# Performance work log

Measured on AMD Instinct MI355X. Metric: run time of the kernel, lower is better.

## Reference

```python
import jax, jax.numpy as jnp
import numpy as np

N, S, E, H = 2, 2048, 1024, 16
D = E // H  # size_per_head


def setup_inputs() -> dict:
    key = jax.random.key(0)
    ks = jax.random.split(key, 12)
    s = 0.02
    inp = {
        "key":   jax.random.normal(ks[0], (N, S, E), jnp.float32),
        "value": jax.random.normal(ks[1], (N, S, E), jnp.float32),
        "query": jax.random.normal(ks[2], (N, S, E), jnp.float32),
        # causal mask (S, T): 1 = attend, 0 = masked
        "mask":  jnp.tril(jnp.ones((S, S), jnp.int32)),
        "Wk": jax.random.normal(ks[3], (E, E), jnp.float32) * s,
        "bk": jnp.zeros((E,), jnp.float32),
        "Wq": jax.random.normal(ks[4], (E, E), jnp.float32) * s,
        "bq": jnp.zeros((E,), jnp.float32),
        "Wv": jax.random.normal(ks[5], (E, E), jnp.float32) * s,
        "bv": jnp.zeros((E,), jnp.float32),
        "Wp": jax.random.normal(ks[6], (E, E), jnp.float32) * s,
        "bp": jnp.zeros((E,), jnp.float32),
    }
    return inp


def _heads(x, W, b):
    # (N, L, E) -> (N, H, L, D)
    n, l, _ = x.shape
    y = x @ W.T + b
    return y.reshape(n, l, H, D).transpose(0, 2, 1, 3)


def reference(key, value, query, mask, Wk, bk, Wq, bq, Wv, bv, Wp, bp):
    q = _heads(query, Wq, bq)  # (N, H, S, D)
    k = _heads(key,   Wk, bk)  # (N, H, T, D)
    v = _heads(value, Wv, bv)  # (N, H, T, D)
    scale = 1.0 / jnp.sqrt(jnp.float32(D))
    scores = jnp.einsum("bhsd,bhtd->bhst", q, k) * scale  # (N, H, S, T)
    scores = jnp.where(mask == 0, jnp.float32(-1e12), scores)
    probs = jax.nn.softmax(scores, axis=-1)
    ctx = jnp.einsum("bhst,bhtd->bhsd", probs, v)  # (N, H, S, D)
    ctx = ctx.transpose(0, 2, 1, 3).reshape(query.shape[0], -1, E)  # (N, S, E)
    return ctx @ Wp.T + bp
```

## Files before the change

kernel.cpp:

```cpp
#include <hip/hip_runtime.h>
#include <hip/hip_bf16.h>
#include <math.h>

constexpr int N_B = 2;
constexpr int S_LEN = 2048;
constexpr int E_DIM = 1024;
constexpr int H_NUM = 16;
constexpr int D_HEAD = 64;
constexpr int M_ROWS = N_B * S_LEN;

#define Q_SCALE 0.180336880263082f

typedef __attribute__((ext_vector_type(8))) short bf16x8;
typedef __attribute__((ext_vector_type(4))) float f32x4;

__device__ __forceinline__ short f2bs(float x) {
    __hip_bfloat16 h = __float2bfloat16(x);
    return *reinterpret_cast<short*>(&h);
}

__device__ __forceinline__ void async_lds16(const void* g, void* l) {
    __builtin_amdgcn_global_load_lds(
        (const __attribute__((address_space(1))) unsigned int*)g,
        (__attribute__((address_space(3))) unsigned int*)l, 16, 0, 0);
}

__global__ __launch_bounds__(256) void cast_kernel(
    const float* __restrict__ a0, const float* __restrict__ a1, const float* __restrict__ a2,
    const float* __restrict__ a3, const float* __restrict__ a4, const float* __restrict__ a5,
    const float* __restrict__ a6,
    short* __restrict__ b0, short* __restrict__ b1, short* __restrict__ b2,
    short* __restrict__ b3, short* __restrict__ b4, short* __restrict__ b5,
    short* __restrict__ b6, int n8_in, int n8_w)
{
    const int y = blockIdx.y;
    const float* s; short* d;
    switch (y) {
        case 0: s = a0; d = b0; break;
        case 1: s = a1; d = b1; break;
        case 2: s = a2; d = b2; break;
        case 3: s = a3; d = b3; break;
        case 4: s = a4; d = b4; break;
        case 5: s = a5; d = b5; break;
        default: s = a6; d = b6; break;
    }
    const int n8 = (y < 3) ? n8_in : n8_w;
    const int i = blockIdx.x * 256 + threadIdx.x;
    if (i >= n8) return;
    const float4* f4 = (const float4*)s;
    const float4 a = f4[i * 2], b = f4[i * 2 + 1];
    bf16x8 o;
    o[0] = f2bs(a.x); o[1] = f2bs(a.y); o[2] = f2bs(a.z); o[3] = f2bs(a.w);
    o[4] = f2bs(b.x); o[5] = f2bs(b.y); o[6] = f2bs(b.z); o[7] = f2bs(b.w);
    *(bf16x8*)(d + (size_t)i * 8) = o;
}

__device__ __forceinline__ void gemm128_core(
    const short* __restrict__ A, const short* __restrict__ W,
    const float* __restrict__ bias, float* __restrict__ outf,
    short* __restrict__ outb, int mode, float scale, short* As, short* Bs)
{
    constexpr int K = E_DIM;
    const int tid = threadIdx.x;
    const int wave = tid >> 6, lane = tid & 63;
    const int l16 = lane & 15, quad = lane >> 4;
    const int wm = wave >> 1, wn = wave & 1;
    const int m0 = blockIdx.y * 128, n0 = blockIdx.x * 128;
    const int lr = lane >> 2;
    const int lc = (lane & 3) * 8;

    const short* Arow0 = A + (size_t)(m0 + wave * 16 + lr) * K + lc;
    const short* Arow1 = A + (size_t)(m0 + (wave + 4) * 16 + lr) * K + lc;
    const short* Wrow0 = W + (size_t)(n0 + wave * 16 + lr) * K + lc;
    const short* Wrow1 = W + (size_t)(n0 + (wave + 4) * 16 + lr) * K + lc;
    short* Asw0 = As + wave * 512; short* Asw1 = As + (wave + 4) * 512;
    short* Bsw0 = Bs + wave * 512; short* Bsw1 = Bs + (wave + 4) * 512;

    f32x4 acc[4][4];
    #pragma unroll
    for (int i = 0; i < 4; ++i)
        #pragma unroll
        for (int j = 0; j < 4; ++j)
            acc[i][j] = (f32x4){0.f, 0.f, 0.f, 0.f};

    for (int k0 = 0; k0 < K; k0 += 32) {
        async_lds16(Arow0 + k0, Asw0);
        async_lds16(Arow1 + k0, Asw1);
        async_lds16(Wrow0 + k0, Bsw0);
        async_lds16(Wrow1 + k0, Bsw1);
        __syncthreads();

        bf16x8 af[4], bfr[4];
        #pragma unroll
        for (int i = 0; i < 4; ++i) {
            af[i]  = *(const bf16x8*)(As + (wm * 64 + i * 16 + l16) * 32 + quad * 8);
            bfr[i] = *(const bf16x8*)(Bs + (wn * 64 + i * 16 + l16) * 32 + quad * 8);
        }
        #pragma unroll
        for (int mi = 0; mi < 4; ++mi)
            #pragma unroll
            for (int ni = 0; ni < 4; ++ni)
                acc[mi][ni] = __builtin_amdgcn_mfma_f32_16x16x32_bf16(
                    af[mi], bfr[ni], acc[mi][ni], 0, 0, 0);
        __syncthreads();
    }

    #pragma unroll
    for (int ni = 0; ni < 4; ++ni) {
        const int n = n0 + wn * 64 + ni * 16 + l16;
        const float bv = bias[n];
        #pragma unroll
        for (int mi = 0; mi < 4; ++mi) {
            #pragma unroll
            for (int r = 0; r < 4; ++r) {
                const int m = m0 + wm * 64 + mi * 16 + quad * 4 + r;
                const float val = (acc[mi][ni][r] + bv) * scale;
                if (mode == 0) {
                    outf[(size_t)m * E_DIM + n] = val;
                } else {
                    const int nb = m >> 11, s = m & 2047;
                    const int hh = n >> 6, d = n & 63;
                    if (mode == 1)
                        outb[(((size_t)(nb * H_NUM + hh)) * S_LEN + s) * D_HEAD + d] = f2bs(val);
                    else
                        outb[(((size_t)(nb * H_NUM + hh)) * D_HEAD + d) * S_LEN + s] = f2bs(val);
                }
            }
        }
    }
}

__global__ __launch_bounds__(256) void qkv_gemm_kernel(
    const short* __restrict__ qA, const short* __restrict__ kA, const short* __restrict__ vA,
    const short* __restrict__ Wq, const short* __restrict__ Wk, const short* __restrict__ Wv,
    const float* __restrict__ bq, const float* __restrict__ bk, const float* __restrict__ bv,
    short* __restrict__ oq, short* __restrict__ ok, short* __restrict__ ov)
{
    __shared__ short As[128 * 32];
    __shared__ short Bs[128 * 32];
    const int z = blockIdx.z;
    const short* A = z == 0 ? qA : z == 1 ? kA : vA;
    const short* W = z == 0 ? Wq : z == 1 ? Wk : Wv;
    const float* b = z == 0 ? bq : z == 1 ? bk : bv;
    short* o       = z == 0 ? oq : z == 1 ? ok : ov;
    gemm128_core(A, W, b, nullptr, o, z == 2 ? 2 : 1,
                 z == 0 ? Q_SCALE : 1.0f, As, Bs);
}

__global__ __launch_bounds__(256) void proj_gemm_kernel(
    const short* __restrict__ A, const short* __restrict__ W,
    const float* __restrict__ b, float* __restrict__ out)
{
    __shared__ short As[128 * 32];
    __shared__ short Bs[128 * 32];
    gemm128_core(A, W, b, out, nullptr, 0, 1.0f, As, Bs);
}

__global__ __launch_bounds__(256, 2) void fattn_kernel(
    const short* __restrict__ qg, const short* __restrict__ kg,
    const short* __restrict__ vtg, short* __restrict__ ctx)
{
    const int nh   = blockIdx.x & 31;
    const int pidx = blockIdx.x >> 5;
    const int tid  = threadIdx.x;
    const int wave = tid >> 6, lane = tid & 63;
    const int l16  = lane & 15, quad = lane >> 4;

    __shared__ short Ks[2][64 * 64];
    __shared__ short Vs[2][64 * 64];
    __shared__ short Ps[4][16 * 72];

    const size_t hb = (size_t)nh * S_LEN * D_HEAD;
    const short* kb  = kg + hb;
    const short* vtb = vtg + hb;
    const int nb = nh >> 4, h = nh & 15;

    const int srow = lane >> 3;
    const int schk = ((lane & 7) ^ srow) * 8;
    const int sw   = l16 & 7;

    for (int pi = 0; pi < 2; ++pi) {
        const int qt = pi ? (31 - pidx) : pidx;
        const int q0 = qt * 64;
        const int ntile = qt + 1;

        const short* qp = qg + hb + (size_t)(q0 + wave * 16 + l16) * D_HEAD;
        const bf16x8 qf0 = *(const bf16x8*)(qp + quad * 8);
        const bf16x8 qf1 = *(const bf16x8*)(qp + 32 + quad * 8);

        f32x4 O[4];
        float m_r[4], l_r[4];
        #pragma unroll
        for (int r = 0; r < 4; ++r) {
            O[r] = (f32x4){0.f, 0.f, 0.f, 0.f};
            m_r[r] = -1e30f;
            l_r[r] = 0.f;
        }
        const int qmaxw = q0 + wave * 16 + 15;

        __syncthreads();
        #pragma unroll
        for (int j = 0; j < 2; ++j) {
            const int r0 = wave * 16 + j * 8;
            async_lds16(kb + (size_t)(r0 + srow) * D_HEAD + schk, &Ks[0][r0 * 64]);
            async_lds16(vtb + (size_t)(r0 + srow) * S_LEN + schk, &Vs[0][r0 * 64]);
        }

        for (int it = 0; it < ntile; ++it) {
            const int buf = it & 1;
            const int t0 = it * 64;
            __syncthreads();

            if (it + 1 < ntile) {
                const int t1 = t0 + 64;
                #pragma unroll
                for (int j = 0; j < 2; ++j) {
                    const int r0 = wave * 16 + j * 8;
                    async_lds16(kb + (size_t)(t1 + r0 + srow) * D_HEAD + schk,
                                &Ks[buf ^ 1][r0 * 64]);
                    async_lds16(vtb + (size_t)(r0 + srow) * S_LEN + t1 + schk,
                                &Vs[buf ^ 1][r0 * 64]);
                }
            }

            const bool isdiag = (it == qt);

            float sc[4][4];
            #pragma unroll
            for (int c = 0; c < 4; ++c) {
                const bool act = !isdiag || (c <= wave);
                if (act) {
                    const int t = c * 16 + l16;
                    const bf16x8 k0 = *(const bf16x8*)(&Ks[buf][t * 64 + ((quad ^ sw) * 8)]);
                    const bf16x8 k1 = *(const bf16x8*)(&Ks[buf][t * 64 + (((quad + 4) ^ sw) * 8)]);
                    f32x4 s = {0.f, 0.f, 0.f, 0.f};
                    s = __builtin_amdgcn_mfma_f32_16x16x32_bf16(qf0, k0, s, 0, 0, 0);
                    s = __builtin_amdgcn_mfma_f32_16x16x32_bf16(qf1, k1, s, 0, 0, 0);
                    if (isdiag) {
                        const int tg = t0 + c * 16 + l16;
                        #pragma unroll
                        for (int r = 0; r < 4; ++r) {
                            const int qrow = q0 + wave * 16 + quad * 4 + r;
                            sc[c][r] = (tg <= qrow) ? s[r] : -1e30f;
                        }
                    } else {
                        #pragma unroll
                        for (int r = 0; r < 4; ++r) sc[c][r] = s[r];
                    }
                } else {
                    #pragma unroll
                    for (int r = 0; r < 4; ++r) sc[c][r] = -1e30f;
                }
            }

            float rmax[4];
            #pragma unroll
            for (int r = 0; r < 4; ++r)
                rmax[r] = fmaxf(fmaxf(sc[0][r], sc[1][r]), fmaxf(sc[2][r], sc[3][r]));
            #pragma unroll
            for (int off = 1; off < 16; off <<= 1)
                #pragma unroll
                for (int r = 0; r < 4; ++r)
                    rmax[r] = fmaxf(rmax[r], __shfl_xor(rmax[r], off));

            float alpha[4], p[4][4], rsum[4];
            #pragma unroll
            for (int r = 0; r < 4; ++r) {
                const float mn = fmaxf(m_r[r], rmax[r]);
                alpha[r] = __builtin_amdgcn_exp2f(m_r[r] - mn);
                m_r[r] = mn;
                #pragma unroll
                for (int c = 0; c < 4; ++c)
                    p[c][r] = __builtin_amdgcn_exp2f(sc[c][r] - mn);
                rsum[r] = (p[0][r] + p[1][r]) + (p[2][r] + p[3][r]);
            }
            #pragma unroll
            for (int off = 1; off < 16; off <<= 1)
                #pragma unroll
                for (int r = 0; r < 4; ++r)
                    rsum[r] += __shfl_xor(rsum[r], off);
            #pragma unroll
            for (int r = 0; r < 4; ++r)
                l_r[r] = l_r[r] * alpha[r] + rsum[r];

            #pragma unroll
            for (int c = 0; c < 4; ++c)
                #pragma unroll
                for (int r = 0; r < 4; ++r)
                    Ps[wave][(quad * 4 + r) * 72 + c * 16 + l16] = f2bs(p[c][r]);

            #pragma unroll
            for (int nt = 0; nt < 4; ++nt)
                #pragma unroll
                for (int r = 0; r < 4; ++r)
                    O[nt][r] *= alpha[r];

            const bf16x8 pf0 = *(const bf16x8*)(&Ps[wave][l16 * 72 + quad * 8]);
            const bf16x8 pf1 = *(const bf16x8*)(&Ps[wave][l16 * 72 + 32 + quad * 8]);
            #pragma unroll
            for (int nt = 0; nt < 4; ++nt) {
                const int d = nt * 16 + l16;
                const bf16x8 v0 = *(const bf16x8*)(&Vs[buf][d * 64 + ((quad ^ sw) * 8)]);
                const bf16x8 v1 = *(const bf16x8*)(&Vs[buf][d * 64 + (((quad + 4) ^ sw) * 8)]);
                O[nt] = __builtin_amdgcn_mfma_f32_16x16x32_bf16(pf0, v0, O[nt], 0, 0, 0);
                O[nt] = __builtin_amdgcn_mfma_f32_16x16x32_bf16(pf1, v1, O[nt], 0, 0, 0);
            }
        }

        float inv[4];
        #pragma unroll
        for (int r = 0; r < 4; ++r) inv[r] = 1.f / l_r[r];
        #pragma unroll
        for (int nt = 0; nt < 4; ++nt) {
            #pragma unroll
            for (int r = 0; r < 4; ++r) {
                const int qrow = q0 + wave * 16 + quad * 4 + r;
                const int d = nt * 16 + l16;
                ctx[((size_t)(nb * S_LEN + qrow)) * E_DIM + h * D_HEAD + d] =
                    f2bs(O[nt][r] * inv[r]);
            }
        }
    }
}

extern "C" void kernel_launch(void* const* d_in, const int* in_sizes, int n_in,
                              void* d_out, int out_size, void* d_ws, size_t ws_size,
                              hipStream_t stream) {
    const float* key   = (const float*)d_in[0];
    const float* value = (const float*)d_in[1];
    const float* query = (const float*)d_in[2];
    const float* Wk = (const float*)d_in[4];
    const float* bk = (const float*)d_in[5];
    const float* Wq = (const float*)d_in[6];
    const float* bq = (const float*)d_in[7];
    const float* Wv = (const float*)d_in[8];
    const float* bv = (const float*)d_in[9];
    const float* Wp = (const float*)d_in[10];
    const float* bp = (const float*)d_in[11];

    const size_t ielems = (size_t)M_ROWS * E_DIM;
    const size_t welems = (size_t)E_DIM * E_DIM;
    char* ws = (char*)d_ws;
    short* qib = (short*)(ws);
    short* kib = (short*)(ws + 8  * 1024 * 1024);
    short* vib = (short*)(ws + 16 * 1024 * 1024);
    short* Wqb = (short*)(ws + 24 * 1024 * 1024);
    short* Wkb = (short*)(ws + 26 * 1024 * 1024);
    short* Wvb = (short*)(ws + 28 * 1024 * 1024);
    short* Wpb = (short*)(ws + 30 * 1024 * 1024);
    short* qb  = (short*)(ws + 32 * 1024 * 1024);
    short* kb  = (short*)(ws + 40 * 1024 * 1024);
    short* vbt = (short*)(ws + 48 * 1024 * 1024);
    short* ctx = (short*)(ws + 56 * 1024 * 1024);
    float* out = (float*)d_out;

    cast_kernel<<<dim3((int)(ielems / 8 / 256), 7), 256, 0, stream>>>(
        query, key, value, Wq, Wk, Wv, Wp,
        qib, kib, vib, Wqb, Wkb, Wvb, Wpb,
        (int)(ielems / 8), (int)(welems / 8));

    qkv_gemm_kernel<<<dim3(E_DIM / 128, M_ROWS / 128, 3), 256, 0, stream>>>(
        qib, kib, vib, Wqb, Wkb, Wvb, bq, bk, bv, qb, kb, vbt);

    fattn_kernel<<<dim3(H_NUM * N_B * 16), 256, 0, stream>>>(qb, kb, vbt, ctx);

    proj_gemm_kernel<<<dim3(E_DIM / 128, M_ROWS / 128), 256, 0, stream>>>(
        ctx, Wpb, bp, out);
}
```

Before: 260.8 us.

## Double-buffer GEMM loads, shrink proj tile, transpose attention MFMA for per-lane rows

The GEMM core now double-buffers its LDS tiles, issuing the async global-to-LDS loads for the next K slice before computing on the current one, and drops one barrier per iteration. The projection GEMM uses a 64-row tile so more blocks are launched. The attention kernel swaps MFMA operand order so each lane owns one query row: the row max and sum need only two cross-lane shuffles, the diagonal mask is simpler, and P and ctx are written as packed 8-byte stores. In exchange, the GEMM kernels use twice the LDS, and the narrower proj tile reuses each loaded W tile across fewer rows.

```diff
diff --git a/kernel.cpp b/kernel.cpp
--- a/kernel.cpp
+++ b/kernel.cpp
@@ -17,6 +17,10 @@
 __device__ __forceinline__ short f2bs(float x) {
     __hip_bfloat16 h = __float2bfloat16(x);
     return *reinterpret_cast<short*>(&h);
+}
+__device__ __forceinline__ unsigned int pk2(float a, float b) {
+    return (unsigned int)(unsigned short)f2bs(a) |
+           ((unsigned int)(unsigned short)f2bs(b) << 16);
 }
 
 __device__ __forceinline__ void async_lds16(const void* g, void* l) {
@@ -55,54 +59,70 @@
     *(bf16x8*)(d + (size_t)i * 8) = o;
 }
 
-__device__ __forceinline__ void gemm128_core(
+template <int TM>
+__device__ __forceinline__ void gemm_core(
     const short* __restrict__ A, const short* __restrict__ W,
     const float* __restrict__ bias, float* __restrict__ outf,
     short* __restrict__ outb, int mode, float scale, short* As, short* Bs)
 {
     constexpr int K = E_DIM;
+    constexpr int MI = TM / 32;
     const int tid = threadIdx.x;
     const int wave = tid >> 6, lane = tid & 63;
     const int l16 = lane & 15, quad = lane >> 4;
     const int wm = wave >> 1, wn = wave & 1;
-    const int m0 = blockIdx.y * 128, n0 = blockIdx.x * 128;
+    const int m0 = blockIdx.y * TM, n0 = blockIdx.x * 128;
     const int lr = lane >> 2;
     const int lc = (lane & 3) * 8;
 
     const short* Arow0 = A + (size_t)(m0 + wave * 16 + lr) * K + lc;
-    const short* Arow1 = A + (size_t)(m0 + (wave + 4) * 16 + lr) * K + lc;
+    const short* Arow1 = A + (size_t)(m0 + ((TM == 128 ? wave + 4 : wave)) * 16 + lr) * K + lc;
     const short* Wrow0 = W + (size_t)(n0 + wave * 16 + lr) * K + lc;
     const short* Wrow1 = W + (size_t)(n0 + (wave + 4) * 16 + lr) * K + lc;
-    short* Asw0 = As + wave * 512; short* Asw1 = As + (wave + 4) * 512;
-    short* Bsw0 = Bs + wave * 512; short* Bsw1 = Bs + (wave + 4) * 512;
-
-    f32x4 acc[4][4];
+
+    f32x4 acc[MI][4];
     #pragma unroll
-    for (int i = 0; i < 4; ++i)
+    for (int i = 0; i < MI; ++i)
         #pragma unroll
         for (int j = 0; j < 4; ++j)
             acc[i][j] = (f32x4){0.f, 0.f, 0.f, 0.f};
 
+    {
+        short* Ab = As; short* Bb = Bs;
+        async_lds16(Arow0, Ab + wave * 512);
+        if (TM == 128) async_lds16(Arow1, Ab + (wave + 4) * 512);
+        async_lds16(Wrow0, Bb + wave * 512);
+        async_lds16(Wrow1, Bb + (wave + 4) * 512);
+    }
+
     for (int k0 = 0; k0 < K; k0 += 32) {
-        async_lds16(Arow0 + k0, Asw0);
-        async_lds16(Arow1 + k0, Asw1);
-        async_lds16(Wrow0 + k0, Bsw0);
-        async_lds16(Wrow1 + k0, Bsw1);
+        const int b = (k0 >> 5) & 1;
+        short* Ab = As + b * (TM * 32);
+        short* Bb = Bs + b * (128 * 32);
         __syncthreads();
 
-        bf16x8 af[4], bfr[4];
-        #pragma unroll
-        for (int i = 0; i < 4; ++i) {
-            af[i]  = *(const bf16x8*)(As + (wm * 64 + i * 16 + l16) * 32 + quad * 8);
-            bfr[i] = *(const bf16x8*)(Bs + (wn * 64 + i * 16 + l16) * 32 + quad * 8);
-        }
-        #pragma unroll
-        for (int mi = 0; mi < 4; ++mi)
+        if (k0 + 32 < K) {
+            short* An = As + (b ^ 1) * (TM * 32);
+            short* Bn = Bs + (b ^ 1) * (128 * 32);
+            async_lds16(Arow0 + k0 + 32, An + wave * 512);
+            if (TM == 128) async_lds16(Arow1 + k0 + 32, An + (wave + 4) * 512);
+            async_lds16(Wrow0 + k0 + 32, Bn + wave * 512);
+            async_lds16(Wrow1 + k0 + 32, Bn + (wave + 4) * 512);
+        }
+
+        bf16x8 af[MI], bfr[4];
+        #pragma unroll
+        for (int i = 0; i < MI; ++i)
+            af[i] = *(const bf16x8*)(Ab + (wm * (TM / 2) + i * 16 + l16) * 32 + quad * 8);
+        #pragma unroll
+        for (int j = 0; j < 4; ++j)
+            bfr[j] = *(const bf16x8*)(Bb + (wn * 64 + j * 16 + l16) * 32 + quad * 8);
+        #pragma unroll
+        for (int mi = 0; mi < MI; ++mi)
             #pragma unroll
             for (int ni = 0; ni < 4; ++ni)
                 acc[mi][ni] = __builtin_amdgcn_mfma_f32_16x16x32_bf16(
                     af[mi], bfr[ni], acc[mi][ni], 0, 0, 0);
-        __syncthreads();
     }
 
     #pragma unroll
@@ -110,10 +130,10 @@
         const int n = n0 + wn * 64 + ni * 16 + l16;
         const float bv = bias[n];
         #pragma unroll
-        for (int mi = 0; mi < 4; ++mi) {
+        for (int mi = 0; mi < MI; ++mi) {
             #pragma unroll
             for (int r = 0; r < 4; ++r) {
-                const int m = m0 + wm * 64 + mi * 16 + quad * 4 + r;
+                const int m = m0 + wm * (TM / 2) + mi * 16 + quad * 4 + r;
                 const float val = (acc[mi][ni][r] + bv) * scale;
                 if (mode == 0) {
                     outf[(size_t)m * E_DIM + n] = val;
@@ -136,24 +156,24 @@
     const float* __restrict__ bq, const float* __restrict__ bk, const float* __restrict__ bv,
     short* __restrict__ oq, short* __restrict__ ok, short* __restrict__ ov)
 {
-    __shared__ short As[128 * 32];
-    __shared__ short Bs[128 * 32];
+    __shared__ short As[2 * 128 * 32];
+    __shared__ short Bs[2 * 128 * 32];
     const int z = blockIdx.z;
     const short* A = z == 0 ? qA : z == 1 ? kA : vA;
     const short* W = z == 0 ? Wq : z == 1 ? Wk : Wv;
     const float* b = z == 0 ? bq : z == 1 ? bk : bv;
     short* o       = z == 0 ? oq : z == 1 ? ok : ov;
-    gemm128_core(A, W, b, nullptr, o, z == 2 ? 2 : 1,
-                 z == 0 ? Q_SCALE : 1.0f, As, Bs);
+    gemm_core<128>(A, W, b, nullptr, o, z == 2 ? 2 : 1,
+                   z == 0 ? Q_SCALE : 1.0f, As, Bs);
 }
 
 __global__ __launch_bounds__(256) void proj_gemm_kernel(
     const short* __restrict__ A, const short* __restrict__ W,
     const float* __restrict__ b, float* __restrict__ out)
 {
-    __shared__ short As[128 * 32];
-    __shared__ short Bs[128 * 32];
-    gemm128_core(A, W, b, out, nullptr, 0, 1.0f, As, Bs);
+    __shared__ short As[2 * 64 * 32];
+    __shared__ short Bs[2 * 128 * 32];
+    gemm_core<64>(A, W, b, out, nullptr, 0, 1.0f, As, Bs);
 }
 
 __global__ __launch_bounds__(256, 2) void fattn_kernel(
@@ -183,20 +203,16 @@
         const int qt = pi ? (31 - pidx) : pidx;
         const int q0 = qt * 64;
         const int ntile = qt + 1;
-
-        const short* qp = qg + hb + (size_t)(q0 + wave * 16 + l16) * D_HEAD;
+        const int q = q0 + wave * 16 + l16;
+
+        const short* qp = qg + hb + (size_t)q * D_HEAD;
         const bf16x8 qf0 = *(const bf16x8*)(qp + quad * 8);
         const bf16x8 qf1 = *(const bf16x8*)(qp + 32 + quad * 8);
 
         f32x4 O[4];
-        float m_r[4], l_r[4];
-        #pragma unroll
-        for (int r = 0; r < 4; ++r) {
-            O[r] = (f32x4){0.f, 0.f, 0.f, 0.f};
-            m_r[r] = -1e30f;
-            l_r[r] = 0.f;
-        }
-        const int qmaxw = q0 + wave * 16 + 15;
+        #pragma unroll
+        for (int nt = 0; nt < 4; ++nt) O[nt] = (f32x4){0.f, 0.f, 0.f, 0.f};
+        float m_s = -1e30f, l_s = 0.f;
 
         __syncthreads();
         #pragma unroll
@@ -230,19 +246,16 @@
             for (int c = 0; c < 4; ++c) {
                 const bool act = !isdiag || (c <= wave);
                 if (act) {
-                    const int t = c * 16 + l16;
-                    const bf16x8 k0 = *(const bf16x8*)(&Ks[buf][t * 64 + ((quad ^ sw) * 8)]);
-                    const bf16x8 k1 = *(const bf16x8*)(&Ks[buf][t * 64 + (((quad + 4) ^ sw) * 8)]);
+                    const int trow = c * 16 + l16;
+                    const bf16x8 k0 = *(const bf16x8*)(&Ks[buf][trow * 64 + ((quad ^ sw) * 8)]);
+                    const bf16x8 k1 = *(const bf16x8*)(&Ks[buf][trow * 64 + (((quad + 4) ^ sw) * 8)]);
                     f32x4 s = {0.f, 0.f, 0.f, 0.f};
-                    s = __builtin_amdgcn_mfma_f32_16x16x32_bf16(qf0, k0, s, 0, 0, 0);
-                    s = __builtin_amdgcn_mfma_f32_16x16x32_bf16(qf1, k1, s, 0, 0, 0);
-                    if (isdiag) {
-                        const int tg = t0 + c * 16 + l16;
+                    s = __builtin_amdgcn_mfma_f32_16x16x32_bf16(k0, qf0, s, 0, 0, 0);
+                    s = __builtin_amdgcn_mfma_f32_16x16x32_bf16(k1, qf1, s, 0, 0, 0);
+                    if (isdiag && c == wave) {
                         #pragma unroll
-                        for (int r = 0; r < 4; ++r) {
-                            const int qrow = q0 + wave * 16 + quad * 4 + r;
-                            sc[c][r] = (tg <= qrow) ? s[r] : -1e30f;
-                        }
+                        for (int r = 0; r < 4; ++r)
+                            sc[c][r] = (4 * quad + r <= l16) ? s[r] : -1e30f;
                     } else {
                         #pragma unroll
                         for (int r = 0; r < 4; ++r) sc[c][r] = s[r];
@@ -253,72 +266,67 @@
                 }
             }
 
-            float rmax[4];
-            #pragma unroll
-            for (int r = 0; r < 4; ++r)
-                rmax[r] = fmaxf(fmaxf(sc[0][r], sc[1][r]), fmaxf(sc[2][r], sc[3][r]));
-            #pragma unroll
-            for (int off = 1; off < 16; off <<= 1)
-                #pragma unroll
-                for (int r = 0; r < 4; ++r)
-                    rmax[r] = fmaxf(rmax[r], __shfl_xor(rmax[r], off));
-
-            float alpha[4], p[4][4], rsum[4];
-            #pragma unroll
-            for (int r = 0; r < 4; ++r) {
-                const float mn = fmaxf(m_r[r], rmax[r]);
-                alpha[r] = __builtin_amdgcn_exp2f(m_r[r] - mn);
-                m_r[r] = mn;
-                #pragma unroll
-                for (int c = 0; c < 4; ++c)
-                    p[c][r] = __builtin_amdgcn_exp2f(sc[c][r] - mn);
-                rsum[r] = (p[0][r] + p[1][r]) + (p[2][r] + p[3][r]);
-            }
-            #pragma unroll
-            for (int off = 1; off < 16; off <<= 1)
-                #pragma unroll
-                for (int r = 0; r < 4; ++r)
-                    rsum[r] += __shfl_xor(rsum[r], off);
-            #pragma unroll
-            for (int r = 0; r < 4; ++r)
-                l_r[r] = l_r[r] * alpha[r] + rsum[r];
-
+            float mloc = sc[0][0];
             #pragma unroll
             for (int c = 0; c < 4; ++c)
                 #pragma unroll
                 for (int r = 0; r < 4; ++r)
-                    Ps[wave][(quad * 4 + r) * 72 + c * 16 + l16] = f2bs(p[c][r]);
+                    mloc = fmaxf(mloc, sc[c][r]);
+            mloc = fmaxf(mloc, __shfl_xor(mloc, 16));
+            mloc = fmaxf(mloc, __shfl_xor(mloc, 32));
+
+            const float mn = fmaxf(m_s, mloc);
+            const float alpha = __builtin_amdgcn_exp2f(m_s - mn);
+            m_s = mn;
+
+            float p[4][4];
+            float sl = 0.f;
+            #pragma unroll
+            for (int c = 0; c < 4; ++c)
+                #pragma unroll
+                for (int r = 0; r < 4; ++r) {
+                    p[c][r] = __builtin_amdgcn_exp2f(sc[c][r] - mn);
+                    sl += p[c][r];
+                }
+            sl += __shfl_xor(sl, 16);
+            sl += __shfl_xor(sl, 32);
+            l_s = l_s * alpha + sl;
+
+            short* prow = &Ps[wave][l16 * 72];
+            #pragma unroll
+            for (int c = 0; c < 4; ++c) {
+                uint2 w;
+                w.x = pk2(p[c][0], p[c][1]);
+                w.y = pk2(p[c][2], p[c][3]);
+                *(uint2*)(prow + c * 16 + quad * 4) = w;
+            }
 
             #pragma unroll
             for (int nt = 0; nt < 4; ++nt)
                 #pragma unroll
                 for (int r = 0; r < 4; ++r)
-                    O[nt][r] *= alpha[r];
-
-            const bf16x8 pf0 = *(const bf16x8*)(&Ps[wave][l16 * 72 + quad * 8]);
-            const bf16x8 pf1 = *(const bf16x8*)(&Ps[wave][l16 * 72 + 32 + quad * 8]);
+                    O[nt][r] *= alpha;
+
+            const bf16x8 pf0 = *(const bf16x8*)(prow + quad * 8);
+            const bf16x8 pf1 = *(const bf16x8*)(prow + 32 + quad * 8);
             #pragma unroll
             for (int nt = 0; nt < 4; ++nt) {
-                const int d = nt * 16 + l16;
-                const bf16x8 v0 = *(const bf16x8*)(&Vs[buf][d * 64 + ((quad ^ sw) * 8)]);
-                const bf16x8 v1 = *(const bf16x8*)(&Vs[buf][d * 64 + (((quad + 4) ^ sw) * 8)]);
-                O[nt] = __builtin_amdgcn_mfma_f32_16x16x32_bf16(pf0, v0, O[nt], 0, 0, 0);
-                O[nt] = __builtin_amdgcn_mfma_f32_16x16x32_bf16(pf1, v1, O[nt], 0, 0, 0);
-            }
-        }
-
-        float inv[4];
-        #pragma unroll
-        for (int r = 0; r < 4; ++r) inv[r] = 1.f / l_r[r];
+                const int drow = nt * 16 + l16;
+                const bf16x8 v0 = *(const bf16x8*)(&Vs[buf][drow * 64 + ((quad ^ sw) * 8)]);
+                const bf16x8 v1 = *(const bf16x8*)(&Vs[buf][drow * 64 + (((quad + 4) ^ sw) * 8)]);
+                O[nt] = __builtin_amdgcn_mfma_f32_16x16x32_bf16(v0, pf0, O[nt], 0, 0, 0);
+                O[nt] = __builtin_amdgcn_mfma_f32_16x16x32_bf16(v1, pf1, O[nt], 0, 0, 0);
+            }
+        }
+
+        const float inv = 1.f / l_s;
+        short* obase = ctx + ((size_t)(nb * S_LEN + q)) * E_DIM + h * D_HEAD;
         #pragma unroll
         for (int nt = 0; nt < 4; ++nt) {
-            #pragma unroll
-            for (int r = 0; r < 4; ++r) {
-                const int qrow = q0 + wave * 16 + quad * 4 + r;
-                const int d = nt * 16 + l16;
-                ctx[((size_t)(nb * S_LEN + qrow)) * E_DIM + h * D_HEAD + d] =
-                    f2bs(O[nt][r] * inv[r]);
-            }
+            uint2 w;
+            w.x = pk2(O[nt][0] * inv, O[nt][1] * inv);
+            w.y = pk2(O[nt][2] * inv, O[nt][3] * inv);
+            *(uint2*)(obase + nt * 16 + quad * 4) = w;
         }
     }
 }
@@ -364,6 +372,6 @@
 
     fattn_kernel<<<dim3(H_NUM * N_B * 16), 256, 0, stream>>>(qb, kb, vbt, ctx);
 
-    proj_gemm_kernel<<<dim3(E_DIM / 128, M_ROWS / 128), 256, 0, stream>>>(
+    proj_gemm_kernel<<<dim3(E_DIM / 128, M_ROWS / 64), 256, 0, stream>>>(
         ctx, Wpb, bp, out);
 }
```

Result: faster. 239.1 us (-8.3%).
